# Kernel optimization log

Measured on AMD Instinct MI355X. Metric: run time of the kernel, lower is better.

Reference implementation:

```python
import jax, jax.numpy as jnp
import numpy as np


def _conv3d(x, w, stride, pad):
    return jax.lax.conv_general_dilated(
        x, w, window_strides=stride, padding=[(p, p) for p in pad],
        dimension_numbers=('NCDHW', 'OIDHW', 'NCDHW'))


def _bn(x, g, b, eps=1e-5):
    # BatchNorm3d in training mode: batch statistics over (N, D, H, W)
    m = x.mean((0, 2, 3, 4), keepdims=True)
    v = ((x - m) ** 2).mean((0, 2, 3, 4), keepdims=True)
    return (x - m) * jax.lax.rsqrt(v + eps) * g.reshape(1, -1, 1, 1, 1) + b.reshape(1, -1, 1, 1, 1)


def _lrelu(x):
    return jnp.where(x >= 0, x, 0.2 * x)


def _deform_conv3d(x, off, w, stride, pad, n_off_groups):
    # Deformable conv3d: offsets predict per-output-location (dz,dy,dx) shifts for
    # every kernel tap, shared across channel groups of size C//n_off_groups.
    B, C, D, H, W = x.shape
    O, _, kd, kh, kw = w.shape
    K = kd * kh * kw
    sd, sh, sw = stride
    pd, ph, pw = pad
    Do = (D + 2 * pd - kd) // sd + 1
    Ho = (H + 2 * ph - kh) // sh + 1
    Wo = (W + 2 * pw - kw) // sw + 1
    G = n_off_groups
    Cg = C // G
    # offset layout: [B, G, K, 3(dz,dy,dx), Do, Ho, Wo]
    off = off.reshape(B, G, K, 3, Do, Ho, Wo)
    kz, ky, kx = jnp.meshgrid(jnp.arange(kd), jnp.arange(kh), jnp.arange(kw), indexing='ij')
    bz = (jnp.arange(Do) * sd - pd).astype(x.dtype)[:, None, None]
    by = (jnp.arange(Ho) * sh - ph).astype(x.dtype)[None, :, None]
    bx = (jnp.arange(Wo) * sw - pw).astype(x.dtype)[None, None, :]
    kb = lambda a: a.reshape(-1).astype(x.dtype)[None, None, :, None, None, None]
    pz = off[:, :, :, 0] + bz + kb(kz)   # [B,G,K,Do,Ho,Wo]
    py = off[:, :, :, 1] + by + kb(ky)
    px = off[:, :, :, 2] + bx + kb(kx)
    z0, y0, x0 = jnp.floor(pz), jnp.floor(py), jnp.floor(px)
    fz, fy, fx = pz - z0, py - y0, px - x0
    xg = x.reshape(B, G, Cg, D * H * W)
    acc = jnp.zeros((B, G, Cg, K, Do, Ho, Wo), x.dtype)
    for cz in (0, 1):
        for cy in (0, 1):
            for cx in (0, 1):
                zc, yc, xc = z0 + cz, y0 + cy, x0 + cx
                wgt = ((fz if cz else 1 - fz) * (fy if cy else 1 - fy) * (fx if cx else 1 - fx))
                valid = ((zc >= 0) & (zc <= D - 1) & (yc >= 0) & (yc <= H - 1)
                         & (xc >= 0) & (xc <= W - 1)).astype(x.dtype)
                zi = jnp.clip(zc, 0, D - 1).astype(jnp.int32)
                yi = jnp.clip(yc, 0, H - 1).astype(jnp.int32)
                xi = jnp.clip(xc, 0, W - 1).astype(jnp.int32)
                idx = ((zi * H + yi) * W + xi).reshape(B, G, 1, -1)
                v = jnp.take_along_axis(xg, jnp.broadcast_to(idx, (B, G, Cg, idx.shape[-1])), axis=3)
                acc = acc + (wgt * valid)[:, :, None] * v.reshape(B, G, Cg, K, Do, Ho, Wo)
    val = acc.reshape(B, C, K, Do, Ho, Wo)
    return jnp.einsum('bckdhw,ock->bodhw', val, w.reshape(O, C, K))


def setup_inputs() -> dict:
    key = jax.random.key(0)
    ks = jax.random.split(key, 24)
    f32 = jnp.float32
    p = lambda k, shape, s=0.05: jax.random.normal(k, shape, f32) * s
    gb = lambda k, c: (1.0 + 0.05 * jax.random.normal(k, (c,), f32),
                       0.05 * jax.random.normal(jax.random.fold_in(k, 1), (c,), f32))
    g2, b2 = gb(ks[8], 64)
    g3, b3 = gb(ks[9], 128)
    g4, b4 = gb(ks[10], 256)
    g5, b5 = gb(ks[11], 512)
    g6, b6 = gb(ks[12], 512)
    return {
        'input': jax.random.normal(ks[0], (64, 3, 8, 128, 128), f32),
        'w1': p(ks[1], (32, 3, 4, 4, 4)),
        'w2': p(ks[2], (64, 32, 2, 4, 4)),
        'w3': p(ks[3], (128, 64, 2, 4, 4)),
        'w4': p(ks[4], (256, 128, 1, 4, 4)),
        'w_off': p(ks[5], (192, 256, 1, 4, 4), 0.01),
        'w5': p(ks[6], (512, 256, 1, 4, 4)),
        'w6': p(ks[7], (512, 512, 1, 4, 4)),
        'g2': g2, 'b2': b2, 'g3': g3, 'b3': b3, 'g4': g4, 'b4': b4,
        'g5': g5, 'b5': b5, 'g6': g6, 'b6': b6,
    }


def reference(input, w1, w2, w3, w4, w_off, w5, w6,
              g2, b2, g3, b3, g4, b4, g5, b5, g6, b6):
    encs = []
    out = _lrelu(_conv3d(input, w1, (2, 2, 2), (1, 1, 1)))          # norm_1 unused in forward
    encs.append(out)
    out = _lrelu(_bn(_conv3d(out, w2, (1, 2, 2), (0, 1, 1)), g2, b2))
    encs.append(out)
    out = _lrelu(_bn(_conv3d(out, w3, (1, 2, 2), (0, 1, 1)), g3, b3))
    encs.append(out)
    out = _lrelu(_bn(_conv3d(out, w4, (1, 2, 2), (0, 1, 1)), g4, b4))
    encs.append(out)
    off = _conv3d(out, w_off, (1, 2, 2), (0, 1, 1))
    out = _lrelu(_bn(_deform_conv3d(out, off, w5, (1, 2, 2), (0, 1, 1), 4), g5, b5))
    encs.append(out)
    out = _lrelu(_bn(_conv3d(out, w6, (1, 1, 1), (0, 0, 0)), g6, b6))
    encs.append(out)
    return tuple(encs)
```

## Files before the change

### kernel.cpp

```cpp
#include <hip/hip_runtime.h>
#include <hip/hip_bf16.h>
#include <cstdint>

typedef short bf16x8 __attribute__((ext_vector_type(8)));
typedef float f32x4 __attribute__((ext_vector_type(4)));

__device__ __forceinline__ float lrelu_f(float y) { return y >= 0.f ? y : 0.2f * y; }
__device__ __forceinline__ float b2f(unsigned short u) {
    union { unsigned int i; float f; } v; v.i = ((unsigned int)u) << 16; return v.f;
}
__device__ __forceinline__ unsigned short f2b(float f) {
    union { unsigned int i; float f; } v; v.f = f;
    unsigned int r = v.i + 0x7FFFu + ((v.i >> 16) & 1u);
    return (unsigned short)(r >> 16);
}

__global__ __launch_bounds__(256) void xin_cl_k(const float* __restrict__ x,
                                                unsigned short* __restrict__ xc)
{
    int i = blockIdx.x * 256 + threadIdx.x;
    int c = i & 3, w = (i >> 2) & 127, h = (i >> 9) & 127, d = (i >> 16) & 7, b = i >> 19;
    float v = (c < 3) ? x[(((size_t)b * 3 + c) * 8 + d) * 16384 + h * 128 + w] : 0.f;
    xc[i] = f2b(v);
}

__global__ __launch_bounds__(256) void repack_all(
    const float* __restrict__ w1, const float* __restrict__ w2,
    const float* __restrict__ w3, const float* __restrict__ w4,
    const float* __restrict__ w_off, const float* __restrict__ w5,
    const float* __restrict__ w6, unsigned short* __restrict__ wp)
{
    long i = (long)blockIdx.x * 256 + threadIdx.x;
    const float* src; int Cin, Tap, Cip; long rel;
    if (i < 8192)         { src = w1;    Cin = 3;   Tap = 64; Cip = 4;   rel = i; }
    else if (i < 73728)   { src = w2;    Cin = 32;  Tap = 32; Cip = 32;  rel = i - 8192; }
    else if (i < 335872)  { src = w3;    Cin = 64;  Tap = 32; Cip = 64;  rel = i - 73728; }
    else if (i < 860160)  { src = w4;    Cin = 128; Tap = 16; Cip = 128; rel = i - 335872; }
    else if (i < 1646592) { src = w_off; Cin = 256; Tap = 16; Cip = 256; rel = i - 860160; }
    else if (i < 3743744) { src = w5;    Cin = 256; Tap = 16; Cip = 256; rel = i - 1646592; }
    else                  { src = w6;    Cin = 512; Tap = 16; Cip = 512; rel = i - 3743744; }
    int c = (int)(rel % Cip);
    long t1 = rel / Cip;
    int t = (int)(t1 % Tap);
    long o = t1 / Tap;
    wp[i] = (c < Cin) ? f2b(src[((size_t)o * Cin + c) * Tap + t]) : (unsigned short)0;
}

template<int TM, int BN, int AMODE, int EPI>
__global__ __launch_bounds__(TM * 2) void igemm(
    const unsigned short* __restrict__ A, const unsigned short* __restrict__ Bw,
    void* __restrict__ Cout, float* __restrict__ sums,
    int M, int N, int K, int klen,
    int Ci, int Di, int Hi, int Wi,
    int kd, int kh, int kw,
    int sd, int sh_, int sw_, int pd, int ph_, int pw_,
    int Do, int Ho, int Wo)
{
    constexpr int NT = TM * 2;
    constexpr int NF = BN / 32;
    constexpr int WN = 16 * NF;
    constexpr int NBU = (BN * 4 + NT - 1) / NT;
    constexpr int NAU = (AMODE == 2) ? 4 : 2;
    constexpr int ASTR = 4 * TM * 8;
    constexpr int BSTR = 4 * BN * 8;
    __shared__ __align__(16) unsigned short As[2][4][TM][8];
    __shared__ __align__(16) unsigned short Bs[2][4][BN][8];
    __shared__ float redbuf[(EPI == 4) ? 2 * BN : 1];
    const int tid = threadIdx.x;
    const int m0 = blockIdx.x * TM;
    const int n0 = blockIdx.y * BN;
    const int k0 = blockIdx.z * klen;
    const int kend = min(K, k0 + klen);
    unsigned short* const As0 = &As[0][0][0][0];
    unsigned short* const Bs0 = &Bs[0][0][0][0];

    size_t bsrc[NBU];
    int boff[NBU];
#pragma unroll
    for (int i = 0; i < NBU; ++i) {
        int u = tid + i * NT;
        int row = u >> 2, s = u & 3;
        if (BN * 4 >= NT || u < BN * 4) {
            bsrc[i] = (size_t)(n0 + row) * K + s * 8;
            boff[i] = (s * BN + row) * 8;
        }
    }

    size_t asz[2];
    int asrc[NAU];
    unsigned long long amask[NAU];
    int aoff[NAU];

    if constexpr (AMODE == 0) {
#pragma unroll
        for (int i = 0; i < 2; ++i) {
            int u = tid + i * NT;
            int r = u >> 2, s = u & 3;
            asz[i] = (size_t)(m0 + r) * K + s * 8;
            aoff[i] = (s * TM + r) * 8;
        }
    } else {
#pragma unroll
        for (int i = 0; i < NAU; ++i) {
            int u = tid + i * NT;
            int r = (AMODE == 2) ? (u >> 3) : (u >> 2);
            int m = m0 + r;
            int ow = m % Wo; int t1 = m / Wo;
            int oh = t1 % Ho; t1 /= Ho;
            int od = t1 % Do; int b = t1 / Do;
            int id0 = od * sd - pd, ih0 = oh * sh_ - ph_, iw0 = ow * sw_ - pw_;
            unsigned long long xm = 0ull, yx = 0ull, mask = 0ull;
            for (int p = 0; p < kw; ++p) if ((unsigned)(iw0 + p) < (unsigned)Wi) xm |= 1ull << p;
            for (int p = 0; p < kh; ++p) if ((unsigned)(ih0 + p) < (unsigned)Hi) yx |= xm << (p * kw);
            for (int p = 0; p < kd; ++p) if ((unsigned)(id0 + p) < (unsigned)Di) mask |= yx << (p * kh * kw);
            amask[i] = mask;
            int bsp = ((b * Di + id0) * Hi + ih0) * Wi + iw0;
            if constexpr (AMODE == 1) {
                int s = u & 3;
                asrc[i] = bsp * Ci + s * 8;
                aoff[i] = (s * TM + r) * 8;
            } else {
                int j = u & 7;
                asrc[i] = (bsp + (j >> 2) * Wi + (j & 3)) * 4;
                aoff[i] = ((j >> 1) * TM + r) * 8 + (j & 1) * 4;
            }
        }
    }

    f32x4 acc[4][NF];
#pragma unroll
    for (int i = 0; i < 4; ++i)
#pragma unroll
        for (int j = 0; j < NF; ++j) acc[i][j] = (f32x4){0.f, 0.f, 0.f, 0.f};

    const int lane = tid & 63, wv = tid >> 6;
    const int wm = wv >> 1, wn = wv & 1;
    const int kg = lane >> 4, fr = lane & 15;

    int c0 = 0, kx = 0, ky = 0, tap = 0, doff = 0;
    if constexpr (AMODE == 1) {
        c0 = k0 % Ci;
        tap = k0 / Ci;
        kx = tap % kw;
        int t2 = tap / kw;
        ky = t2 % kh;
        int kz = t2 / kh;
        doff = (kz * Hi + ky) * Wi + kx;
    }
    auto advance = [&]() {
        c0 += 32;
        if (c0 >= Ci) {
            c0 = 0; ++tap; ++kx; ++doff;
            if (kx == kw) {
                kx = 0; doff += Wi - kw; ++ky;
                if (ky == kh) { ky = 0; doff += (Hi - kh) * Wi; }
            }
        }
    };

    for (int k = k0; k < kend; k += 64) {
#pragma unroll
        for (int i = 0; i < NBU; ++i)
            if (BN * 4 >= NT || tid + i * NT < BN * 4) {
                uint4 v0 = *(const uint4*)&Bw[bsrc[i] + k];
                uint4 v1 = *(const uint4*)&Bw[bsrc[i] + k + 32];
                *(uint4*)(Bs0 + boff[i]) = v0;
                *(uint4*)(Bs0 + BSTR + boff[i]) = v1;
            }
        if constexpr (AMODE == 0) {
#pragma unroll
            for (int i = 0; i < 2; ++i) {
                uint4 v0 = *(const uint4*)&A[asz[i] + k];
                uint4 v1 = *(const uint4*)&A[asz[i] + k + 32];
                *(uint4*)(As0 + aoff[i]) = v0;
                *(uint4*)(As0 + ASTR + aoff[i]) = v1;
            }
        } else if constexpr (AMODE == 1) {
            int t0 = tap, d0 = doff * Ci + c0;
            advance();
            int t1 = tap, d1 = doff * Ci + c0;
            advance();
#pragma unroll
            for (int i = 0; i < 2; ++i) {
                uint4 v0 = {0u, 0u, 0u, 0u}, v1 = {0u, 0u, 0u, 0u};
                if ((amask[i] >> t0) & 1ull) v0 = *(const uint4*)&A[(size_t)(asrc[i] + d0)];
                if ((amask[i] >> t1) & 1ull) v1 = *(const uint4*)&A[(size_t)(asrc[i] + d1)];
                *(uint4*)(As0 + aoff[i]) = v0;
                *(uint4*)(As0 + ASTR + aoff[i]) = v1;
            }
        } else {
            int kz = k >> 6;
            int U0 = kz * (Hi * Wi) * 4;
            int U1 = U0 + 2 * Wi * 4;
            int tap0 = k >> 2;
#pragma unroll
            for (int i = 0; i < 4; ++i) {
                int j = (tid + i * NT) & 7;
                uint2 v0 = {0u, 0u}, v1 = {0u, 0u};
                if ((amask[i] >> (tap0 + j)) & 1ull)
                    v0 = *(const uint2*)&A[(size_t)(asrc[i] + U0)];
                if ((amask[i] >> (tap0 + 8 + j)) & 1ull)
                    v1 = *(const uint2*)&A[(size_t)(asrc[i] + U1)];
                *(uint2*)(As0 + aoff[i]) = v0;
                *(uint2*)(As0 + ASTR + aoff[i]) = v1;
            }
        }
        __syncthreads();
#pragma unroll
        for (int kb = 0; kb < 2; ++kb) {
            bf16x8 af[4], bfr[NF];
#pragma unroll
            for (int mi = 0; mi < 4; ++mi)
                af[mi] = *(const bf16x8*)&As[kb][kg][wm * 64 + mi * 16 + fr][0];
#pragma unroll
            for (int ni = 0; ni < NF; ++ni)
                bfr[ni] = *(const bf16x8*)&Bs[kb][kg][wn * WN + ni * 16 + fr][0];
#pragma unroll
            for (int mi = 0; mi < 4; ++mi)
#pragma unroll
                for (int ni = 0; ni < NF; ++ni)
                    acc[mi][ni] = __builtin_amdgcn_mfma_f32_16x16x32_bf16(af[mi], bfr[ni], acc[mi][ni], 0, 0, 0);
        }
        __syncthreads();
    }

    if constexpr (EPI == 4) {
        for (int j = tid; j < 2 * BN; j += NT) redbuf[j] = 0.f;
        __syncthreads();
    }
    const int rb = m0 + wm * 64 + (lane >> 4) * 4;
    const int cb = n0 + wn * WN + fr;
    float p1[NF], p2[NF];
    if constexpr (EPI == 4) {
#pragma unroll
        for (int ni = 0; ni < NF; ++ni) { p1[ni] = 0.f; p2[ni] = 0.f; }
    }
#pragma unroll
    for (int mi = 0; mi < 4; ++mi)
#pragma unroll
        for (int rg = 0; rg < 4; ++rg) {
            size_t rowbase = (size_t)(rb + mi * 16 + rg) * N;
#pragma unroll
            for (int ni = 0; ni < NF; ++ni) {
                size_t idx = rowbase + cb + ni * 16;
                float vv = acc[mi][ni][rg];
                if constexpr (EPI == 0) ((unsigned short*)Cout)[idx] = f2b(vv);
                else if constexpr (EPI == 1) ((float*)Cout)[idx] = vv;
                else if constexpr (EPI == 2) atomicAdd((float*)Cout + idx, vv);
                else if constexpr (EPI == 3 || EPI == 5) ((unsigned short*)Cout)[idx] = f2b(lrelu_f(vv));
                else {
                    ((unsigned short*)Cout)[idx] = f2b(vv);
                    p1[ni] += vv; p2[ni] += vv * vv;
                }
            }
        }
    if constexpr (EPI == 4) {
#pragma unroll
        for (int ni = 0; ni < NF; ++ni) {
            int cl = wn * WN + ni * 16 + fr;
            atomicAdd(&redbuf[cl], p1[ni]);
            atomicAdd(&redbuf[BN + cl], p2[ni]);
        }
        __syncthreads();
        for (int j = tid; j < 2 * BN; j += NT) {
            int gcol = (j < BN) ? (n0 + j) : (N + n0 + j - BN);
            atomicAdd(&sums[gcol], redbuf[j]);
        }
    }
    if constexpr (EPI == 5) {
#pragma unroll
        for (int mi = 0; mi < 4; ++mi) {
            int mr = rb + mi * 16;
            int b = mr >> 14, ssp = mr & 16383;
            float4 f;
            f.x = lrelu_f(acc[mi][0][0]);
            f.y = lrelu_f(acc[mi][0][1]);
            f.z = lrelu_f(acc[mi][0][2]);
            f.w = lrelu_f(acc[mi][0][3]);
            *(float4*)&sums[((size_t)(b * 32 + cb)) * 16384 + ssp] = f;
        }
    }
}

__global__ __launch_bounds__(256) void f2b_sums(const float* __restrict__ in,
                                                unsigned short* __restrict__ o,
                                                float* __restrict__ sums,
                                                long totalSlots, int C)
{
    const int tid = threadIdx.x;
    long gid = (long)blockIdx.x * 256 + tid;
    long stride = (long)gridDim.x * 256;
    float s1[8], s2[8];
#pragma unroll
    for (int j = 0; j < 8; ++j) { s1[j] = 0.f; s2[j] = 0.f; }
    for (long s = gid; s < totalSlots; s += stride) {
        float4 a = *(const float4*)&in[s * 8];
        float4 b = *(const float4*)&in[s * 8 + 4];
        float f[8] = {a.x, a.y, a.z, a.w, b.x, b.y, b.z, b.w};
        unsigned short u[8];
#pragma unroll
        for (int j = 0; j < 8; ++j) { u[j] = f2b(f[j]); s1[j] += f[j]; s2[j] += f[j] * f[j]; }
        *(uint4*)&o[s * 8] = *(uint4*)u;
    }
    __shared__ float r1[2048], r2[2048];
#pragma unroll
    for (int j = 0; j < 8; ++j) { r1[tid * 8 + j] = s1[j]; r2[tid * 8 + j] = s2[j]; }
    __syncthreads();
    int G = C >> 3;
    for (int c = tid; c < C; c += 256) {
        int grp = c >> 3, j = c & 7;
        float a = 0.f, b = 0.f;
        for (int th = grp; th < 256; th += G) { a += r1[th * 8 + j]; b += r2[th * 8 + j]; }
        atomicAdd(&sums[c], a);
        atomicAdd(&sums[C + c], b);
    }
}

__global__ __launch_bounds__(256) void bn_fin(float* __restrict__ sums,
                                              const float* __restrict__ g, const float* __restrict__ bt,
                                              float* __restrict__ sc, float* __restrict__ sh,
                                              int C, float invcnt)
{
    int c = blockIdx.x * 256 + threadIdx.x;
    if (c >= C) return;
    float mean = sums[c] * invcnt;
    float var = sums[C + c] * invcnt - mean * mean;
    float rs = rsqrtf(var + 1e-5f);
    float scl = g[c] * rs;
    sc[c] = scl;
    sh[c] = bt[c] - mean * scl;
    sums[c] = 0.f;
    sums[C + c] = 0.f;
}

__global__ __launch_bounds__(256) void bn_apply_t(
    unsigned short* __restrict__ x, const float* __restrict__ sc, const float* __restrict__ sh,
    float* __restrict__ outN, int C, int TC, int S)
{
    __shared__ __align__(16) float T[64][68];
    const int tid = threadIdx.x;
    const long m0 = (long)blockIdx.x * 64;
    const int c0 = blockIdx.y * TC;
    const int spr = TC >> 3;
    const int lg = (spr == 8) ? 3 : 2;
    const int tot = 64 * spr;
    for (int u = tid; u < tot; u += 256) {
        int r = u >> lg, sl = u & (spr - 1);
        size_t idx = (size_t)(m0 + r) * C + c0 + sl * 8;
        uint4 v = *(uint4*)&x[idx];
        unsigned short* pv = (unsigned short*)&v;
#pragma unroll
        for (int j = 0; j < 8; ++j) {
            int c = c0 + sl * 8 + j;
            float f = b2f(pv[j]);
            f = lrelu_f(f * sc[c] + sh[c]);
            pv[j] = f2b(f);
            T[sl * 8 + j][r] = f;
        }
        *(uint4*)&x[idx] = v;
    }
    __syncthreads();
    const int tpc = 256 / TC;
    const int rpt = 64 / tpc;
    int cl = tid / tpc;
    int r0 = (tid % tpc) * rpt;
    int c = c0 + cl;
    if ((S & 63) == 0) {
        long b = m0 / S;
        long s0 = m0 - b * S;
        float* op = outN + ((size_t)b * C + c) * S + s0 + r0;
        for (int r = 0; r < rpt; r += 4)
            *(float4*)(op + r) = *(float4*)&T[cl][r0 + r];
    } else {
        for (int r = 0; r < rpt; ++r) {
            long m = m0 + r0 + r;
            long b = m / S, s = m - b * S;
            outN[((size_t)b * C + c) * S + s] = T[cl][r0 + r];
        }
    }
}

__global__ __launch_bounds__(256) void deform_val(
    const unsigned short* __restrict__ xcl, const float* __restrict__ offc,
    unsigned short* __restrict__ val)
{
    int bs = blockIdx.x;
    int b = bs >> 5, s = bs & 31;
    int od = s >> 4, oh = (s >> 2) & 3, ow = s & 3;
    __shared__ float cw[64][8];
    __shared__ int cidx[64][8];
    int tid = threadIdx.x;
    if (tid < 64) {
        int gk = tid, k = gk & 15;
        int ky = k >> 2, kx = k & 3;
        const float* op = offc + (size_t)bs * 192 + gk * 3;
        float pz = op[0] + (float)od;
        float py = op[1] + (float)(oh * 2 - 1 + ky);
        float px = op[2] + (float)(ow * 2 - 1 + kx);
        float z0 = floorf(pz), y0 = floorf(py), x0 = floorf(px);
        float fz = pz - z0, fy = py - y0, fx = px - x0;
#pragma unroll
        for (int ci = 0; ci < 8; ++ci) {
            int cz = ci >> 2, cy = (ci >> 1) & 1, cx = ci & 1;
            float zc = z0 + cz, yc = y0 + cy, xc = x0 + cx;
            bool ok = zc >= 0.f && zc <= 1.f && yc >= 0.f && yc <= 7.f && xc >= 0.f && xc <= 7.f;
            int zi = min(max((int)zc, 0), 1);
            int yi = min(max((int)yc, 0), 7);
            int xi = min(max((int)xc, 0), 7);
            float wz = cz ? fz : 1.f - fz;
            float wy = cy ? fy : 1.f - fy;
            float wx = cx ? fx : 1.f - fx;
            cw[gk][ci] = ok ? wz * wy * wx : 0.f;
            cidx[gk][ci] = (zi * 8 + yi) * 8 + xi;
        }
    }
    __syncthreads();
    const unsigned short* xb = xcl + (size_t)b * 128 * 256;
    unsigned short* vo = val + (size_t)bs * 4096;
    for (int j = tid; j < 4096; j += 256) {
        int c = j & 255, tap = j >> 8;
        int gk = ((c >> 6) << 4) | tap;
        float v = 0.f;
#pragma unroll
        for (int i = 0; i < 8; ++i)
            v += cw[gk][i] * b2f(xb[(size_t)cidx[gk][i] * 256 + c]);
        vo[j] = f2b(v);
    }
}

extern "C" void kernel_launch(void* const* d_in, const int* in_sizes, int n_in,
                              void* d_out, int out_size, void* d_ws, size_t ws_size,
                              hipStream_t stream)
{
    (void)in_sizes; (void)n_in; (void)out_size; (void)ws_size;
    const float* x     = (const float*)d_in[0];
    const float* w1    = (const float*)d_in[1];
    const float* w2    = (const float*)d_in[2];
    const float* w3    = (const float*)d_in[3];
    const float* w4    = (const float*)d_in[4];
    const float* w_off = (const float*)d_in[5];
    const float* w5    = (const float*)d_in[6];
    const float* w6    = (const float*)d_in[7];
    const float* g2 = (const float*)d_in[8];  const float* b2 = (const float*)d_in[9];
    const float* g3 = (const float*)d_in[10]; const float* b3 = (const float*)d_in[11];
    const float* g4 = (const float*)d_in[12]; const float* b4 = (const float*)d_in[13];
    const float* g5 = (const float*)d_in[14]; const float* b5 = (const float*)d_in[15];
    const float* g6 = (const float*)d_in[16]; const float* b6 = (const float*)d_in[17];

    float* out = (float*)d_out;
    float* enc0 = out;
    float* enc1 = out + 33554432;
    float* enc2 = out + 46137344;
    float* enc3 = out + 50331648;
    float* enc4 = out + 52428800;
    float* enc5 = out + 53477376;

    char* W = (char*)d_ws;
    unsigned short* wpk  = (unsigned short*)(W + 0);
    unsigned short* w1p  = (unsigned short*)(W + 0);
    unsigned short* w2p  = (unsigned short*)(W + 16384);
    unsigned short* w3p  = (unsigned short*)(W + 147456);
    unsigned short* w4p  = (unsigned short*)(W + 671744);
    unsigned short* wofp = (unsigned short*)(W + 1720320);
    unsigned short* w5p  = (unsigned short*)(W + 3293184);
    unsigned short* w6p  = (unsigned short*)(W + 7487488);
    float* sums          = (float*)(W + 15876096);
    float* sc            = (float*)(W + 15880192);
    float* sh            = (float*)(W + 15882240);
    float* offc          = (float*)(W + 15884288);
    unsigned short* xcl  = (unsigned short*)(W + 17457152);
    unsigned short* e1c  = (unsigned short*)(W + 17457152);
    unsigned short* e2c  = (unsigned short*)(W + 42622976);
    unsigned short* e3c  = (unsigned short*)(W + 51011584);
    unsigned short* e0c  = (unsigned short*)(W + 84566016);
    unsigned short* valb = (unsigned short*)(W + 84566016);
    float* raw5          = (float*)(W + 101343232);
    unsigned short* e4c  = (unsigned short*)(W + 105537536);
    float* raw6          = (float*)(W + 107634688);
    unsigned short* e5c  = (unsigned short*)(W + 107896832);

    hipMemsetAsync(sums, 0, 4096, stream);
    xin_cl_k<<<131072, 256, 0, stream>>>(x, xcl);
    repack_all<<<31008, 256, 0, stream>>>(w1, w2, w3, w4, w_off, w5, w6, wpk);

    igemm<256, 32, 2, 5><<<dim3(4096, 1, 1), 512, 0, stream>>>(
        xcl, w1p, e0c, enc0, 1048576, 32, 256, 256,
        4, 8, 128, 128, 4, 4, 4, 2, 2, 2, 1, 1, 1, 4, 64, 64);

    igemm<256, 64, 1, 4><<<dim3(768, 1, 1), 512, 0, stream>>>(
        e0c, w2p, e1c, sums, 196608, 64, 1024, 1024,
        32, 4, 64, 64, 2, 4, 4, 1, 2, 2, 0, 1, 1, 3, 32, 32);
    bn_fin<<<1, 256, 0, stream>>>(sums, g2, b2, sc, sh, 64, 1.f / 196608.f);
    bn_apply_t<<<dim3(3072, 1), 256, 0, stream>>>(e1c, sc, sh, enc1, 64, 64, 3072);

    igemm<256, 64, 1, 4><<<dim3(128, 2), 512, 0, stream>>>(
        e1c, w3p, e2c, sums, 32768, 128, 2048, 2048,
        64, 3, 32, 32, 2, 4, 4, 1, 2, 2, 0, 1, 1, 2, 16, 16);
    bn_fin<<<1, 256, 0, stream>>>(sums, g3, b3, sc, sh, 128, 1.f / 32768.f);
    bn_apply_t<<<dim3(512, 2), 256, 0, stream>>>(e2c, sc, sh, enc2, 128, 64, 512);

    igemm<128, 64, 1, 4><<<dim3(64, 4), 256, 0, stream>>>(
        e2c, w4p, e3c, sums, 8192, 256, 2048, 2048,
        128, 2, 16, 16, 1, 4, 4, 1, 2, 2, 0, 1, 1, 2, 8, 8);
    bn_fin<<<1, 256, 0, stream>>>(sums, g4, b4, sc, sh, 256, 1.f / 8192.f);
    bn_apply_t<<<dim3(128, 4), 256, 0, stream>>>(e3c, sc, sh, enc3, 256, 64, 128);

    hipMemsetAsync(offc, 0, 1572864, stream);
    igemm<128, 64, 1, 2><<<dim3(16, 3, 8), 256, 0, stream>>>(
        e3c, wofp, offc, nullptr, 2048, 192, 4096, 512,
        256, 2, 8, 8, 1, 4, 4, 1, 2, 2, 0, 1, 1, 2, 4, 4);

    deform_val<<<2048, 256, 0, stream>>>(e3c, offc, valb);
    hipMemsetAsync(raw5, 0, 4194304, stream);
    igemm<128, 64, 0, 2><<<dim3(16, 8, 8), 256, 0, stream>>>(
        valb, w5p, raw5, nullptr, 2048, 512, 4096, 512,
        0, 0, 0, 0, 1, 1, 1, 1, 1, 1, 0, 0, 0, 1, 1, 1);
    f2b_sums<<<256, 256, 0, stream>>>(raw5, e4c, sums, 131072L, 512);
    bn_fin<<<2, 256, 0, stream>>>(sums, g5, b5, sc, sh, 512, 1.f / 2048.f);
    bn_apply_t<<<dim3(32, 8), 256, 0, stream>>>(e4c, sc, sh, enc4, 512, 64, 32);

    hipMemsetAsync(raw6, 0, 262144, stream);
    igemm<128, 64, 0, 2><<<dim3(1, 8, 32), 256, 0, stream>>>(
        e4c, w6p, raw6, nullptr, 128, 512, 8192, 256,
        0, 0, 0, 0, 1, 1, 1, 1, 1, 1, 0, 0, 0, 1, 1, 1);
    f2b_sums<<<32, 256, 0, stream>>>(raw6, e5c, sums, 8192L, 512);
    bn_fin<<<2, 256, 0, stream>>>(sums, g6, b6, sc, sh, 512, 1.f / 128.f);
    bn_apply_t<<<dim3(2, 8), 256, 0, stream>>>(e5c, sc, sh, enc5, 512, 64, 2);
}
```

Before: 553.4 us.

## Double-buffer igemm shared tiles with register prefetch and fuse prep kernels

The implicit-GEMM main loop now loads the next K-slice from global memory into registers while MFMAs run on the current shared-memory buffer. It then writes that slice into the alternate buffer, so each iteration needs one barrier instead of two. This doubles shared memory per block and raises register pressure, which may lower occupancy. The input layout conversion and weight repacking kernels are also merged into one launch to cut launch overhead.

```diff
diff --git a/kernel.cpp b/kernel.cpp
--- a/kernel.cpp
+++ b/kernel.cpp
@@ -15,22 +15,22 @@
     return (unsigned short)(r >> 16);
 }
 
-__global__ __launch_bounds__(256) void xin_cl_k(const float* __restrict__ x,
-                                                unsigned short* __restrict__ xc)
-{
-    int i = blockIdx.x * 256 + threadIdx.x;
-    int c = i & 3, w = (i >> 2) & 127, h = (i >> 9) & 127, d = (i >> 16) & 7, b = i >> 19;
-    float v = (c < 3) ? x[(((size_t)b * 3 + c) * 8 + d) * 16384 + h * 128 + w] : 0.f;
-    xc[i] = f2b(v);
-}
-
-__global__ __launch_bounds__(256) void repack_all(
+__global__ __launch_bounds__(256) void prep_k(
+    const float* __restrict__ x, unsigned short* __restrict__ xc,
     const float* __restrict__ w1, const float* __restrict__ w2,
     const float* __restrict__ w3, const float* __restrict__ w4,
     const float* __restrict__ w_off, const float* __restrict__ w5,
     const float* __restrict__ w6, unsigned short* __restrict__ wp)
 {
-    long i = (long)blockIdx.x * 256 + threadIdx.x;
+    int bid = blockIdx.x;
+    if (bid < 131072) {
+        int i = bid * 256 + threadIdx.x;
+        int c = i & 3, w = (i >> 2) & 127, h = (i >> 9) & 127, d = (i >> 16) & 7, b = i >> 19;
+        float v = (c < 3) ? x[(((size_t)b * 3 + c) * 8 + d) * 16384 + h * 128 + w] : 0.f;
+        xc[i] = f2b(v);
+        return;
+    }
+    long i = (long)(bid - 131072) * 256 + threadIdx.x;
     const float* src; int Cin, Tap, Cip; long rel;
     if (i < 8192)         { src = w1;    Cin = 3;   Tap = 64; Cip = 4;   rel = i; }
     else if (i < 73728)   { src = w2;    Cin = 32;  Tap = 32; Cip = 32;  rel = i - 8192; }
@@ -61,18 +61,16 @@
     constexpr int WN = 16 * NF;
     constexpr int NBU = (BN * 4 + NT - 1) / NT;
     constexpr int NAU = (AMODE == 2) ? 4 : 2;
-    constexpr int ASTR = 4 * TM * 8;
-    constexpr int BSTR = 4 * BN * 8;
-    __shared__ __align__(16) unsigned short As[2][4][TM][8];
-    __shared__ __align__(16) unsigned short Bs[2][4][BN][8];
+    constexpr int AH = 4 * TM * 8;
+    constexpr int BH = 4 * BN * 8;
+    __shared__ __align__(16) unsigned short As[2][8][TM][8];
+    __shared__ __align__(16) unsigned short Bs[2][8][BN][8];
     __shared__ float redbuf[(EPI == 4) ? 2 * BN : 1];
     const int tid = threadIdx.x;
     const int m0 = blockIdx.x * TM;
     const int n0 = blockIdx.y * BN;
     const int k0 = blockIdx.z * klen;
     const int kend = min(K, k0 + klen);
-    unsigned short* const As0 = &As[0][0][0][0];
-    unsigned short* const Bs0 = &Bs[0][0][0][0];
 
     size_t bsrc[NBU];
     int boff[NBU];
@@ -158,22 +156,22 @@
         }
     };
 
-    for (int k = k0; k < kend; k += 64) {
+    uint4 vb0[NBU], vb1[NBU];
+    uint4 va0[2], va1[2];
+    uint2 w0r[4], w1r[4];
+
+    auto ISSUE = [&](int k) {
 #pragma unroll
         for (int i = 0; i < NBU; ++i)
             if (BN * 4 >= NT || tid + i * NT < BN * 4) {
-                uint4 v0 = *(const uint4*)&Bw[bsrc[i] + k];
-                uint4 v1 = *(const uint4*)&Bw[bsrc[i] + k + 32];
-                *(uint4*)(Bs0 + boff[i]) = v0;
-                *(uint4*)(Bs0 + BSTR + boff[i]) = v1;
+                vb0[i] = *(const uint4*)&Bw[bsrc[i] + k];
+                vb1[i] = *(const uint4*)&Bw[bsrc[i] + k + 32];
             }
         if constexpr (AMODE == 0) {
 #pragma unroll
             for (int i = 0; i < 2; ++i) {
-                uint4 v0 = *(const uint4*)&A[asz[i] + k];
-                uint4 v1 = *(const uint4*)&A[asz[i] + k + 32];
-                *(uint4*)(As0 + aoff[i]) = v0;
-                *(uint4*)(As0 + ASTR + aoff[i]) = v1;
+                va0[i] = *(const uint4*)&A[asz[i] + k];
+                va1[i] = *(const uint4*)&A[asz[i] + k + 32];
             }
         } else if constexpr (AMODE == 1) {
             int t0 = tap, d0 = doff * Ci + c0;
@@ -182,11 +180,9 @@
             advance();
 #pragma unroll
             for (int i = 0; i < 2; ++i) {
-                uint4 v0 = {0u, 0u, 0u, 0u}, v1 = {0u, 0u, 0u, 0u};
-                if ((amask[i] >> t0) & 1ull) v0 = *(const uint4*)&A[(size_t)(asrc[i] + d0)];
-                if ((amask[i] >> t1) & 1ull) v1 = *(const uint4*)&A[(size_t)(asrc[i] + d1)];
-                *(uint4*)(As0 + aoff[i]) = v0;
-                *(uint4*)(As0 + ASTR + aoff[i]) = v1;
+                uint4 z = {0u, 0u, 0u, 0u};
+                va0[i] = ((amask[i] >> t0) & 1ull) ? *(const uint4*)&A[(size_t)(asrc[i] + d0)] : z;
+                va1[i] = ((amask[i] >> t1) & 1ull) ? *(const uint4*)&A[(size_t)(asrc[i] + d1)] : z;
             }
         } else {
             int kz = k >> 6;
@@ -196,35 +192,69 @@
 #pragma unroll
             for (int i = 0; i < 4; ++i) {
                 int j = (tid + i * NT) & 7;
-                uint2 v0 = {0u, 0u}, v1 = {0u, 0u};
-                if ((amask[i] >> (tap0 + j)) & 1ull)
-                    v0 = *(const uint2*)&A[(size_t)(asrc[i] + U0)];
-                if ((amask[i] >> (tap0 + 8 + j)) & 1ull)
-                    v1 = *(const uint2*)&A[(size_t)(asrc[i] + U1)];
-                *(uint2*)(As0 + aoff[i]) = v0;
-                *(uint2*)(As0 + ASTR + aoff[i]) = v1;
-            }
-        }
-        __syncthreads();
+                uint2 z = {0u, 0u};
+                w0r[i] = ((amask[i] >> (tap0 + j)) & 1ull) ? *(const uint2*)&A[(size_t)(asrc[i] + U0)] : z;
+                w1r[i] = ((amask[i] >> (tap0 + 8 + j)) & 1ull) ? *(const uint2*)&A[(size_t)(asrc[i] + U1)] : z;
+            }
+        }
+    };
+
+    auto WRITE = [&](int buf) {
+        unsigned short* bb = &Bs[buf][0][0][0];
+        unsigned short* ab = &As[buf][0][0][0];
+#pragma unroll
+        for (int i = 0; i < NBU; ++i)
+            if (BN * 4 >= NT || tid + i * NT < BN * 4) {
+                *(uint4*)(bb + boff[i]) = vb0[i];
+                *(uint4*)(bb + BH + boff[i]) = vb1[i];
+            }
+        if constexpr (AMODE == 2) {
+#pragma unroll
+            for (int i = 0; i < 4; ++i) {
+                *(uint2*)(ab + aoff[i]) = w0r[i];
+                *(uint2*)(ab + AH + aoff[i]) = w1r[i];
+            }
+        } else {
+#pragma unroll
+            for (int i = 0; i < 2; ++i) {
+                *(uint4*)(ab + aoff[i]) = va0[i];
+                *(uint4*)(ab + AH + aoff[i]) = va1[i];
+            }
+        }
+    };
+
+    ISSUE(k0);
+    WRITE(0);
+    __syncthreads();
+    int cur = 0;
+
+    for (int k = k0; k < kend; k += 64) {
+        const bool more = (k + 64 < kend);
+        if (more) ISSUE(k + 64);
 #pragma unroll
         for (int kb = 0; kb < 2; ++kb) {
             bf16x8 af[4], bfr[NF];
 #pragma unroll
             for (int mi = 0; mi < 4; ++mi)
-                af[mi] = *(const bf16x8*)&As[kb][kg][wm * 64 + mi * 16 + fr][0];
+                af[mi] = *(const bf16x8*)&As[cur][kb * 4 + kg][wm * 64 + mi * 16 + fr][0];
 #pragma unroll
             for (int ni = 0; ni < NF; ++ni)
-                bfr[ni] = *(const bf16x8*)&Bs[kb][kg][wn * WN + ni * 16 + fr][0];
+                bfr[ni] = *(const bf16x8*)&Bs[cur][kb * 4 + kg][wn * WN + ni * 16 + fr][0];
 #pragma unroll
             for (int mi = 0; mi < 4; ++mi)
 #pragma unroll
                 for (int ni = 0; ni < NF; ++ni)
                     acc[mi][ni] = __builtin_amdgcn_mfma_f32_16x16x32_bf16(af[mi], bfr[ni], acc[mi][ni], 0, 0, 0);
         }
+        if (more) {
+            WRITE(cur ^ 1);
+            __syncthreads();
+            cur ^= 1;
+        }
+    }
+
+    if constexpr (EPI == 4) {
         __syncthreads();
-    }
-
-    if constexpr (EPI == 4) {
         for (int j = tid; j < 2 * BN; j += NT) redbuf[j] = 0.f;
         __syncthreads();
     }
@@ -480,8 +510,7 @@
     unsigned short* e5c  = (unsigned short*)(W + 107896832);
 
     hipMemsetAsync(sums, 0, 4096, stream);
-    xin_cl_k<<<131072, 256, 0, stream>>>(x, xcl);
-    repack_all<<<31008, 256, 0, stream>>>(w1, w2, w3, w4, w_off, w5, w6, wpk);
+    prep_k<<<162080, 256, 0, stream>>>(x, xcl, w1, w2, w3, w4, w_off, w5, w6, wpk);
 
     igemm<256, 32, 2, 5><<<dim3(4096, 1, 1), 512, 0, stream>>>(
         xcl, w1p, e0c, enc0, 1048576, 32, 256, 256,
```

New measurement: 737.8 us. 1.33x slower.
